# Performance work log

Hardware: AMD Instinct MI355X
Metric: run time of the kernel (lower is better)

Reference implementation:

```python
import jax, jax.numpy as jnp
import numpy as np

B, S, D, H, P = 2, 2048, 512, 8, 10  # batch, seq, d_model, heads, max_relative_position
DH = D // H
SCALE = float(np.sqrt(D))  # module uses sqrt(d_model) in relative branch


def _rel_indices(len_q, len_k, max_rel):
    rq = jnp.arange(len_q)
    rk = jnp.arange(len_k)
    dist = rk[None, :] - rq[:, None]
    return jnp.clip(dist, -max_rel, max_rel) + max_rel  # [len_q, len_k]


def setup_inputs() -> dict:
    key = jax.random.key(0)
    ks = jax.random.split(key, 12)
    init = lambda k, shp, s=0.02: (jax.random.normal(k, shp, dtype=jnp.float32) * s)
    return {
        "q": jax.random.normal(ks[0], (B, S, D), dtype=jnp.float32),
        "k": jax.random.normal(ks[1], (B, S, D), dtype=jnp.float32),
        "v": jax.random.normal(ks[2], (B, S, D), dtype=jnp.float32),
        "mask": jnp.ones((1, 1, S, S), dtype=jnp.int32),  # no-op in original (masked_fill result discarded)
        "Wq": init(ks[3], (D, D)), "bq": init(ks[4], (D,)),
        "Wk": init(ks[5], (D, D)), "bk": init(ks[6], (D,)),
        "Wv": init(ks[7], (D, D)), "bv": init(ks[8], (D,)),
        "W0": init(ks[9], (D, D)), "b0": init(ks[10], (D,)),
        "rel_k_table": init(ks[11], (2 * P + 1, DH), 0.02),
        "rel_v_table": init(jax.random.fold_in(key, 99), (2 * P + 1, DH), 0.02),
    }


def reference(q, k, v, mask, Wq, bq, Wk, bk, Wv, bv, W0, b0, rel_k_table, rel_v_table):
    # Projections (nn.Linear equivalent with weight stored as [in, out])
    query = q @ Wq + bq  # [B,S,D]
    key_ = k @ Wk + bk
    value = v @ Wv + bv

    qh = query.reshape(B, S, H, DH)  # [B,S,H,DH]
    kh = key_.reshape(B, S, H, DH)
    vh = value.reshape(B, S, H, DH)

    idx = _rel_indices(S, S, P)              # [S,S]
    rel_k = rel_k_table[idx]                 # [S,S,DH]
    rel_v = rel_v_table[idx]                 # [S,S,DH]

    normal_scores = jnp.einsum("bqhd,bkhd->bhqk", qh, kh)
    rel_scores = jnp.einsum("bqhd,qkd->bhqk", qh, rel_k)
    # NOTE: original relative branch applies NO softmax; mask is a no-op (masked_fill not in-place)
    scores = (normal_scores + rel_scores) / SCALE  # [B,H,S,S]

    weight1 = jnp.einsum("bhqk,bkhd->bhqd", scores, vh)
    weight2 = jnp.einsum("bhqk,qkd->bhqd", scores, rel_v)
    x = (weight1 + weight2).transpose(0, 2, 1, 3).reshape(B, S, D)
    return x @ W0 + b0
```

## Files before the change

### kernel.cpp

```cpp
#include <hip/hip_runtime.h>
#include <hip/hip_bf16.h>


typedef __attribute__((ext_vector_type(8)))  short  short8;
typedef __attribute__((ext_vector_type(4)))  short  short4v;
typedef __attribute__((ext_vector_type(16))) float  f32x16;
typedef __attribute__((ext_vector_type(8)))  __bf16 bf16x8;

#define DEV static __device__ __forceinline__

constexpr float INV_SCALE = 0.044194173824159216f;

DEV unsigned short f2bs(float f){ __hip_bfloat16 h = __float2bfloat16(f); unsigned short u; __builtin_memcpy(&u,&h,2); return u; }
DEV short f2b(float f){ return (short)f2bs(f); }
DEV float b2f(short s){ unsigned u = ((unsigned)(unsigned short)s)<<16; float f; __builtin_memcpy(&f,&u,4); return f; }
DEV bf16x8 ld8s(const short* p){ return __builtin_bit_cast(bf16x8, *(const short8*)p); }
DEV f32x16 z16(){ f32x16 z;
#pragma unroll
  for (int i=0;i<16;++i) z[i]=0.f;
  return z; }
DEV f32x16 mfma32(bf16x8 a, bf16x8 b, f32x16 c){ return __builtin_amdgcn_mfma_f32_32x32x16_bf16(a,b,c,0,0,0); }

template<bool AF32, bool OUTB16>
DEV void gemm_body(const void* A, const float* W, const float* bias, void* C,
                   int m0, int n0, short* Alds, short* Blds, short* Xt){
  const int tid = threadIdx.x, lane = tid&63, wid = tid>>6, lo5 = lane&31, hi = lane>>5;
  f32x16 acc0 = z16(), acc1 = z16();
  const int rr = tid>>3, c = tid&7;
  const int r2 = tid>>2, c4 = tid&3;
  const int kc = r2>>3, ko = r2&7;

  short8 avreg[4];
  short8 bv0r, bv1r;

  auto loadA = [&](int k0){
#pragma unroll
    for (int p=0;p<4;++p){
      const int row = p*32 + rr;
      if (AF32){
        const float* ap = (const float*)A + (size_t)(m0+row)*512 + k0 + c*8;
        float4 x = *(const float4*)ap; float4 y = *(const float4*)(ap+4);
        avreg[p] = short8{ f2b(x.x),f2b(x.y),f2b(x.z),f2b(x.w),
                           f2b(y.x),f2b(y.y),f2b(y.z),f2b(y.w) };
      } else {
        avreg[p] = *(const short8*)((const short*)A + (size_t)(m0+row)*512 + k0 + c*8);
      }
    }
  };
  auto loadB = [&](int k0){
    const float* wrow = W + (size_t)(k0+r2)*512 + n0 + c4*16;
    float4 f0 = *(const float4*)(wrow);
    float4 f1 = *(const float4*)(wrow+4);
    float4 f2 = *(const float4*)(wrow+8);
    float4 f3 = *(const float4*)(wrow+12);
    bv0r = short8{ f2b(f0.x),f2b(f0.y),f2b(f0.z),f2b(f0.w),
                   f2b(f1.x),f2b(f1.y),f2b(f1.z),f2b(f1.w) };
    bv1r = short8{ f2b(f2.x),f2b(f2.y),f2b(f2.z),f2b(f2.w),
                   f2b(f3.x),f2b(f3.y),f2b(f3.z),f2b(f3.w) };
  };

  loadA(0); loadB(0);
  for (int kt=0; kt<8; ++kt){
    __syncthreads();
    {
#pragma unroll
      for (int p=0;p<4;++p){
        const int row = p*32 + rr;
        *(short8*)&Alds[row*64 + ((c ^ (row&7))*8)] = avreg[p];
      }
#pragma unroll
      for (int e=0;e<16;++e){
        const int n = c4*16 + e;
        const short val = (e<8) ? bv0r[e] : bv1r[e-8];
        Blds[n*64 + ((kc ^ (n&7))*8) + ko] = val;
      }
    }
    __syncthreads();
    if (kt < 7){ loadA((kt+1)*64); loadB((kt+1)*64); }
#pragma unroll
    for (int da=0; da<4; ++da){
      const int arow = wid*32 + lo5;
      bf16x8 af = ld8s(&Alds[arow*64 + (((2*da+hi) ^ (arow&7))*8)]);
      const int b0r = lo5, b1r = 32+lo5;
      bf16x8 bf0 = ld8s(&Blds[b0r*64 + (((2*da+hi) ^ (b0r&7))*8)]);
      bf16x8 bf1 = ld8s(&Blds[b1r*64 + (((2*da+hi) ^ (b1r&7))*8)]);
      acc0 = mfma32(af, bf0, acc0);
      acc1 = mfma32(af, bf1, acc1);
    }
  }
  const float bv0 = bias[n0 + lo5], bv1 = bias[n0 + 32 + lo5];
#pragma unroll
  for (int r=0;r<16;++r){
    const int m = m0 + wid*32 + (r&3) + 8*(r>>2) + 4*hi;
    const float v0 = acc0[r] + bv0, v1 = acc1[r] + bv1;
    if (OUTB16){
      ((short*)C)[(size_t)m*512 + n0 + lo5]      = f2b(v0);
      ((short*)C)[(size_t)m*512 + n0 + 32 + lo5] = f2b(v1);
    } else {
      ((float*)C)[(size_t)m*512 + n0 + lo5]      = v0;
      ((float*)C)[(size_t)m*512 + n0 + 32 + lo5] = v1;
    }
  }
  if (Xt){
    __syncthreads();
#pragma unroll
    for (int r=0;r<16;++r){
      const int ml = wid*32 + (r&3) + 8*(r>>2) + 4*hi;
      Alds[ml*64 + lo5]      = f2b(acc0[r] + bv0);
      Alds[ml*64 + 32 + lo5] = f2b(acc1[r] + bv1);
    }
    __syncthreads();
    const int dh = tid & 63, chq = tid >> 6;
    short* xrow = Xt + (size_t)dh*2048 + chq*32;
#pragma unroll
    for (int cp=0; cp<4; ++cp){
      short8 t;
#pragma unroll
      for (int e=0;e<8;++e) t[e] = Alds[(chq*32 + cp*8 + e)*64 + dh];
      *(short8*)(xrow + cp*8) = t;
    }
  }
}

struct ProjArgs { const float* A[3]; const float* W[3]; const float* bias[3]; short* C[3]; short* XT[3]; };

__global__ __launch_bounds__(256) void proj_gemm(ProjArgs args){
  __shared__ short Alds[128*64];
  __shared__ short Blds[64*64];
  const int z = blockIdx.z;
  const int m0 = blockIdx.x*128, n0 = blockIdx.y*64;
  short* xt = nullptr;
  if (args.XT[z]){
    const int b = m0>>11, h = n0>>6, s0 = m0&2047;
    xt = args.XT[z] + ((size_t)(b*8+h)*64)*2048 + s0;
  }
  gemm_body<true,true>(args.A[z], args.W[z], args.bias[z], args.C[z],
                       m0, n0, Alds, Blds, xt);
}

__global__ __launch_bounds__(256) void out_gemm(const short* A, const float* W, const float* bias, float* C){
  __shared__ short Alds[128*64];
  __shared__ short Blds[64*64];
  gemm_body<false,false>(A, W, bias, C, blockIdx.x*128, blockIdx.y*64, Alds, Blds, nullptr);
}

__global__ __launch_bounds__(256) void kvpfx_kernel(const short* Kp, const short* Vp,
    const short* Kt, const short* Vt, float* KVpart, float* KP, float* VP){
  __shared__ float shmem[4*64*64];
  const int blk = blockIdx.x, tid = threadIdx.x;

  if (blk < 128){
    const int bh = blk>>3, ch = blk&7;
    const int lane = tid&63, wid = tid>>6, lo5 = lane&31, hi = lane>>5;
    const short* Ktb = Kt + (size_t)bh*64*2048;
    const short* Vtb = Vt + (size_t)bh*64*2048;
    f32x16 a00=z16(), a01=z16(), a10=z16(), a11=z16();
    const int sb = ch*256 + wid*64;
    for (int s = sb; s < sb+64; s += 16){
      bf16x8 ka = ld8s(Ktb + (size_t)lo5*2048 + s + hi*8);
      bf16x8 kb = ld8s(Ktb + (size_t)(32+lo5)*2048 + s + hi*8);
      bf16x8 va = ld8s(Vtb + (size_t)lo5*2048 + s + hi*8);
      bf16x8 vb = ld8s(Vtb + (size_t)(32+lo5)*2048 + s + hi*8);
      a00 = mfma32(ka, va, a00);
      a01 = mfma32(ka, vb, a01);
      a10 = mfma32(kb, va, a10);
      a11 = mfma32(kb, vb, a11);
    }
    float (*red)[64][64] = (float(*)[64][64])shmem;
#pragma unroll
    for (int r=0;r<16;++r){
      int ir = (r&3) + 8*(r>>2) + 4*hi;
      red[wid][ir][lo5]        = a00[r];
      red[wid][ir][32+lo5]     = a01[r];
      red[wid][32+ir][lo5]     = a10[r];
      red[wid][32+ir][32+lo5]  = a11[r];
    }
    __syncthreads();
    float* dst = KVpart + (size_t)(bh*8+ch)*4096;
    for (int e = tid; e < 4096; e += 256){
      int j = e>>6, i = e&63;
      dst[e] = red[0][i][j] + red[1][i][j] + red[2][i][j] + red[3][i][j];
    }
  } else {
    const int idx = blk - 128;
    const int bh = idx>>2, z = (idx>>1)&1, dhalf = idx&1;
    const int b = bh>>3, h = bh&7;
    const short* X = (z ? Vp : Kp) + (size_t)b*2048*512 + h*64 + dhalf*32;
    float* P = (z ? VP : KP) + (size_t)bh*2048*64 + dhalf*32;
    const int dg = tid & 3;
    const int ch = tid >> 2;
    float (*tot)[4][8] = (float(*)[4][8])shmem;

    const short* xp = X + (size_t)(ch*32)*512 + dg*8;
    float acc[8];
#pragma unroll
    for (int j=0;j<8;++j) acc[j]=0.f;
    for (int i=0;i<32;++i){
      short8 v = *(const short8*)(xp + (size_t)i*512);
#pragma unroll
      for (int j=0;j<8;++j) acc[j] += b2f(v[j]);
    }
#pragma unroll
    for (int j=0;j<8;++j) tot[ch][dg][j] = acc[j];
    __syncthreads();

    float run[8];
#pragma unroll
    for (int j=0;j<8;++j) run[j]=0.f;
    for (int cc=0; cc<ch; ++cc){
      float4 a = *(const float4*)&tot[cc][dg][0];
      float4 c4 = *(const float4*)&tot[cc][dg][4];
      run[0]+=a.x; run[1]+=a.y; run[2]+=a.z; run[3]+=a.w;
      run[4]+=c4.x; run[5]+=c4.y; run[6]+=c4.z; run[7]+=c4.w;
    }
    float* pp = P + (size_t)(ch*32)*64 + dg*8;
    for (int i=0;i<32;++i){
      short8 v = *(const short8*)(xp + (size_t)i*512);
#pragma unroll
      for (int j=0;j<8;++j) run[j] += b2f(v[j]);
      float4 o0 = { run[0], run[1], run[2], run[3] };
      float4 o1 = { run[4], run[5], run[6], run[7] };
      *(float4*)(pp + (size_t)i*64)     = o0;
      *(float4*)(pp + (size_t)i*64 + 4) = o1;
    }
  }
}

__global__ __launch_bounds__(256) void attn2_kernel(const short* Qp, const short* Kp,
    const short* Vt, const float* KVpart, const float* KP, const float* VP,
    const float* relk_g, const float* relv_g, short* xb){
  const int qt = blockIdx.x, bh = blockIdx.y;
  const int b = bh>>3, h = bh&7;
  const int tid = threadIdx.x, lane = tid&63, wid = tid>>6, lo5 = lane&31, hi = lane>>5;
  const int q0 = qt*128, qw = q0 + wid*32;

  __shared__ float Rq[128*21];
  __shared__ short CS[128*32];
  __shared__ short RVT[64*32];
  __shared__ short KVl[64*64];

  for (int i=tid; i<2048; i+=256) ((int*)CS)[i] = 0;
  for (int i=tid; i<2048; i+=256){
    int d = i>>5, j = i&31;
    RVT[d*32 + (j ^ ((d&3)<<3))] = (j<21) ? f2b(relv_g[j*64+d]) : (short)0;
  }

  {
    const int j = tid>>2, i0 = (tid&3)*16;
    float acc[16];
#pragma unroll
    for (int t=0;t<16;++t) acc[t]=0.f;
#pragma unroll
    for (int c=0;c<8;++c){
      const float* p = KVpart + (size_t)(bh*8+c)*4096 + j*64 + i0;
#pragma unroll
      for (int t4=0;t4<4;++t4){
        float4 v = *(const float4*)(p + t4*4);
        acc[t4*4+0]+=v.x; acc[t4*4+1]+=v.y; acc[t4*4+2]+=v.z; acc[t4*4+3]+=v.w;
      }
    }
#pragma unroll
    for (int half=0; half<2; ++half){
      short8 o;
#pragma unroll
      for (int e=0;e<8;++e) o[e] = f2b(acc[half*8+e]);
      const int chunk = (i0>>3) + half;
      *(short8*)&KVl[j*64 + ((chunk ^ (j&7))*8)] = o;
    }
  }

  bf16x8 qf[4];
  {
    const short* Qrow = Qp + (size_t)(b*2048 + qw + lo5)*512 + h*64 + hi*8;
#pragma unroll
    for (int da=0;da<4;++da) qf[da] = ld8s(Qrow + da*16);
  }

  {
    f32x16 rq = z16();
    const int jr = lo5 <= 20 ? lo5 : 20;
    const float* rp = relk_g + jr*64 + hi*8;
#pragma unroll
    for (int da=0;da<4;++da){
      const float* p = rp + da*16;
      float4 x = *(const float4*)p; float4 y = *(const float4*)(p+4);
      short8 rb = { f2b(x.x),f2b(x.y),f2b(x.z),f2b(x.w), f2b(y.x),f2b(y.y),f2b(y.z),f2b(y.w) };
      rq = mfma32(qf[da], __builtin_bit_cast(bf16x8, rb), rq);
    }
    if (lo5 <= 20){
#pragma unroll
      for (int r=0;r<16;++r){
        int qoff = (r&3) + 8*(r>>2) + 4*hi;
        Rq[(wid*32 + qoff)*21 + lo5] = rq[r];
      }
    }
  }
  __syncthreads();

  const int qrow = wid*32 + lo5;
  const int qg = q0 + qrow;

  f32x16 w1a = z16(), w1b = z16();

  {
#pragma unroll
    for (int c=0;c<4;++c){
      const int r0i = lo5, r1i = 32+lo5, ck = 2*c+hi;
      bf16x8 b0v = ld8s(&KVl[r0i*64 + ((ck ^ (r0i&7))*8)]);
      bf16x8 b1v = ld8s(&KVl[r1i*64 + ((ck ^ (r1i&7))*8)]);
      w1a = mfma32(qf[c], b0v, w1a);
      w1b = mfma32(qf[c], b1v, w1b);
    }
  }

  {
    const short* Vg = Vt + (size_t)bh*64*2048;
#pragma unroll
    for (int c=0;c<4;++c){
      const int kb = qw - 16 + c*16;
      const int kbse = kb + hi*8;
      const int jb = kbse - (qw + lo5) + 10;
      short8 av;
#pragma unroll
      for (int e=0;e<8;++e){
        int j = jb + e, kk = kbse + e;
        int jc = j < 1 ? 1 : (j > 19 ? 19 : j);
        float rv = Rq[qrow*21 + jc];
        bool ok = (j>=1) && (j<=19) && (kk>=0) && (kk<2048);
        av[e] = ok ? f2b(rv) : (short)0;
      }
      bf16x8 af = __builtin_bit_cast(bf16x8, av);
      const int kc = kb < 0 ? 0 : (kb > 2048-16 ? 2048-16 : kb);
      bf16x8 v0 = ld8s(Vg + (size_t)lo5*2048 + kc + hi*8);
      bf16x8 v1 = ld8s(Vg + (size_t)(32+lo5)*2048 + kc + hi*8);
      w1a = mfma32(af, v0, w1a);
      w1b = mfma32(af, v1, w1b);
    }
  }

  {
    const float* VPb = VP + (size_t)bh*2048*64;
    const float vt0 = VPb[(size_t)2047*64 + lo5];
    const float vt1 = VPb[(size_t)2047*64 + 32 + lo5];
#pragma unroll
    for (int r=0;r<16;++r){
      const int q_r = qw + (r&3) + 8*(r>>2) + 4*hi;
      const int ql = q_r - q0;
      const float r0q  = Rq[ql*21 + 0];
      const float r20q = Rq[ql*21 + 20];
      float p0=0.f, p1=0.f, s0=0.f, s1=0.f;
      if (q_r >= 10){
        const float* pr = VPb + (size_t)(q_r-10)*64;
        p0 = pr[lo5]; p1 = pr[32+lo5];
      }
      if (q_r <= 2037){
        const float* sr = VPb + (size_t)(q_r+9)*64;
        s0 = vt0 - sr[lo5]; s1 = vt1 - sr[32+lo5];
      }
      w1a[r] += r0q*p0 + r20q*s0;
      w1b[r] += r0q*p1 + r20q*s1;
    }
  }

  {
    const short* Kg = Kp + (size_t)b*2048*512 + h*64;
#pragma unroll
    for (int t3=0; t3<3; ++t3){
      const int kb = qw - 32 + t3*32;
      if (kb < 0 || kb >= 2048) continue;
      const short* Krow = Kg + (size_t)(kb + lo5)*512 + hi*8;
      f32x16 acc = z16();
#pragma unroll
      for (int da=0;da<4;++da) acc = mfma32(ld8s(Krow + da*16), qf[da], acc);
#pragma unroll
      for (int r=0;r<16;++r){
        const int krow = kb + (r&3) + 8*(r>>2) + 4*hi;
        const int j = krow - qg + 10;
        if (j >= 1 && j <= 19)
          CS[qrow*32 + (j ^ ((qrow&3)<<3))] = f2b(acc[r] + Rq[qrow*21 + j]);
      }
    }
  }

  {
    const int half = tid >> 7, q_loc = tid & 127;
    const int q_g2 = q0 + q_loc;
    const short* Qr = Qp + (size_t)(b*2048 + q_g2)*512 + h*64;
    const float* KPb = KP + (size_t)bh*2048*64;
    float val = 0.f;
    if (half == 0){
      if (q_g2 >= 10){
        const float* Pr = KPb + (size_t)(q_g2-10)*64;
        float dot = 0.f;
#pragma unroll
        for (int ii=0; ii<8; ++ii){
          short8 qv = *(const short8*)(Qr + ii*8);
          float4 p0 = *(const float4*)(Pr + ii*8);
          float4 p1 = *(const float4*)(Pr + ii*8 + 4);
          dot += b2f(qv[0])*p0.x + b2f(qv[1])*p0.y + b2f(qv[2])*p0.z + b2f(qv[3])*p0.w
               + b2f(qv[4])*p1.x + b2f(qv[5])*p1.y + b2f(qv[6])*p1.z + b2f(qv[7])*p1.w;
        }
        val = dot + (float)(q_g2 - 9) * Rq[q_loc*21 + 0];
      }
      CS[q_loc*32 + (0 ^ ((q_loc&3)<<3))] = f2b(val);
    } else {
      if (q_g2 <= 2037){
        const float* Pt = KPb + (size_t)2047*64;
        const float* Pr = KPb + (size_t)(q_g2+9)*64;
        float dot = 0.f;
#pragma unroll
        for (int ii=0; ii<8; ++ii){
          short8 qv = *(const short8*)(Qr + ii*8);
          float4 p0 = *(const float4*)(Pr + ii*8);
          float4 t0 = *(const float4*)(Pt + ii*8);
          float4 p1 = *(const float4*)(Pr + ii*8 + 4);
          float4 t1 = *(const float4*)(Pt + ii*8 + 4);
          dot += b2f(qv[0])*(t0.x-p0.x) + b2f(qv[1])*(t0.y-p0.y)
               + b2f(qv[2])*(t0.z-p0.z) + b2f(qv[3])*(t0.w-p0.w)
               + b2f(qv[4])*(t1.x-p1.x) + b2f(qv[5])*(t1.y-p1.y)
               + b2f(qv[6])*(t1.z-p1.z) + b2f(qv[7])*(t1.w-p1.w);
        }
        val = dot + (float)(2038 - q_g2) * Rq[q_loc*21 + 20];
      }
      CS[q_loc*32 + (20 ^ ((q_loc&3)<<3))] = f2b(val);
    }
  }
  __syncthreads();

  f32x16 w2a = z16(), w2b = z16();
#pragma unroll
  for (int c2=0;c2<2;++c2){
    const int arow = wid*32 + lo5;
    bf16x8 cf  = ld8s(&CS[arow*32 + ((16*c2 + 8*hi) ^ ((arow&3)<<3))]);
    const int d0 = lo5, d1 = 32 + lo5;
    bf16x8 rv0 = ld8s(&RVT[d0*32 + ((16*c2 + 8*hi) ^ ((d0&3)<<3))]);
    bf16x8 rv1 = ld8s(&RVT[d1*32 + ((16*c2 + 8*hi) ^ ((d1&3)<<3))]);
    w2a = mfma32(cf, rv0, w2a);
    w2b = mfma32(cf, rv1, w2b);
  }

#pragma unroll
  for (int r=0;r<16;++r){
    const int q_r = qw + (r&3) + 8*(r>>2) + 4*hi;
    const size_t o = ((size_t)b*2048 + q_r)*512 + h*64;
    xb[o + lo5]      = f2b((w1a[r] + w2a[r]) * INV_SCALE);
    xb[o + 32 + lo5] = f2b((w1b[r] + w2b[r]) * INV_SCALE);
  }
}

extern "C" void kernel_launch(void* const* d_in, const int* in_sizes, int n_in,
                              void* d_out, int out_size, void* d_ws, size_t ws_size,
                              hipStream_t stream) {
  (void)in_sizes; (void)n_in; (void)out_size; (void)ws_size;
  const float* q    = (const float*)d_in[0];
  const float* k    = (const float*)d_in[1];
  const float* v    = (const float*)d_in[2];
  const float* Wq   = (const float*)d_in[4];
  const float* bq   = (const float*)d_in[5];
  const float* Wk   = (const float*)d_in[6];
  const float* bk   = (const float*)d_in[7];
  const float* Wv   = (const float*)d_in[8];
  const float* bv   = (const float*)d_in[9];
  const float* W0   = (const float*)d_in[10];
  const float* b0   = (const float*)d_in[11];
  const float* relk = (const float*)d_in[12];
  const float* relv = (const float*)d_in[13];
  float* out = (float*)d_out;
  char* ws = (char*)d_ws;

  short* Qp  = (short*)(ws + ((size_t) 2<<20));
  short* Kp  = (short*)(ws + ((size_t) 6<<20));
  short* Vp  = (short*)(ws + ((size_t)10<<20));
  short* Vt  = (short*)(ws + ((size_t)14<<20));
  short* Kt  = (short*)(ws + ((size_t)18<<20));
  float* KVpart = (float*)(ws + ((size_t)22<<20));
  float* KP  = (float*)(ws + ((size_t)24<<20));
  float* VP  = (float*)(ws + ((size_t)32<<20));
  short* xb  = (short*)(ws + ((size_t)40<<20));

  ProjArgs pa = { {q, k, v}, {Wq, Wk, Wv}, {bq, bk, bv}, {Qp, Kp, Vp},
                  {nullptr, Kt, Vt} };
  proj_gemm<<<dim3(32,8,3), 256, 0, stream>>>(pa);

  kvpfx_kernel<<<192, 256, 0, stream>>>(Kp, Vp, Kt, Vt, KVpart, KP, VP);

  attn2_kernel<<<dim3(16,16), 256, 0, stream>>>(Qp, Kp, Vt, KVpart, KP, VP, relk, relv, xb);

  out_gemm<<<dim3(32,8), 256, 0, stream>>>(xb, W0, b0, out);
}
```

Baseline: 81.88 us.

## Fuse prefix, attention and output GEMM into one persistent kernel with grid barriers

Merges the three kernels that follow the projection GEMM into a single 256-block kernel. Software grid barriers built on atomic counters replace the kernel boundaries between stages, and the counters are zeroed by a memset before each launch. The goal is to remove launch overhead and the gaps between dependent kernels. In exchange, every block must be co-resident for the barriers to be safe, blocks spin-wait while others finish, and a shared 64KB LDS buffer may reduce occupancy.

```diff
diff --git a/kernel.cpp b/kernel.cpp
--- a/kernel.cpp
+++ b/kernel.cpp
@@ -20,6 +20,19 @@
   for (int i=0;i<16;++i) z[i]=0.f;
   return z; }
 DEV f32x16 mfma32(bf16x8 a, bf16x8 b, f32x16 c){ return __builtin_amdgcn_mfma_f32_32x32x16_bf16(a,b,c,0,0,0); }
+
+DEV void gridbar(unsigned* cnt, unsigned NB){
+  __syncthreads();
+  __threadfence();
+  if (threadIdx.x == 0){
+    __hip_atomic_fetch_add(cnt, 1u, __ATOMIC_ACQ_REL, __HIP_MEMORY_SCOPE_AGENT);
+    while (__hip_atomic_load(cnt, __ATOMIC_ACQUIRE, __HIP_MEMORY_SCOPE_AGENT) < NB){
+      __builtin_amdgcn_s_sleep(2);
+    }
+  }
+  __syncthreads();
+  __threadfence();
+}
 
 template<bool AF32, bool OUTB16>
 DEV void gemm_body(const void* A, const float* W, const float* bias, void* C,
@@ -138,313 +151,325 @@
                        m0, n0, Alds, Blds, xt);
 }
 
-__global__ __launch_bounds__(256) void out_gemm(const short* A, const float* W, const float* bias, float* C){
-  __shared__ short Alds[128*64];
-  __shared__ short Blds[64*64];
-  gemm_body<false,false>(A, W, bias, C, blockIdx.x*128, blockIdx.y*64, Alds, Blds, nullptr);
-}
-
-__global__ __launch_bounds__(256) void kvpfx_kernel(const short* Kp, const short* Vp,
-    const short* Kt, const short* Vt, float* KVpart, float* KP, float* VP){
-  __shared__ float shmem[4*64*64];
+struct TailArgs {
+  const short* Qp; const short* Kp; const short* Vp;
+  const short* Kt; const short* Vt;
+  float* KVpart; float* KP; float* VP;
+  const float* relk; const float* relv;
+  short* xb;
+  const float* W0; const float* b0; float* out;
+  unsigned* cnt;
+};
+
+__global__ __launch_bounds__(256) void tail_kernel(TailArgs a){
+  __shared__ char smem[65536];
   const int blk = blockIdx.x, tid = threadIdx.x;
-
-  if (blk < 128){
-    const int bh = blk>>3, ch = blk&7;
-    const int lane = tid&63, wid = tid>>6, lo5 = lane&31, hi = lane>>5;
-    const short* Ktb = Kt + (size_t)bh*64*2048;
-    const short* Vtb = Vt + (size_t)bh*64*2048;
-    f32x16 a00=z16(), a01=z16(), a10=z16(), a11=z16();
-    const int sb = ch*256 + wid*64;
-    for (int s = sb; s < sb+64; s += 16){
-      bf16x8 ka = ld8s(Ktb + (size_t)lo5*2048 + s + hi*8);
-      bf16x8 kb = ld8s(Ktb + (size_t)(32+lo5)*2048 + s + hi*8);
-      bf16x8 va = ld8s(Vtb + (size_t)lo5*2048 + s + hi*8);
-      bf16x8 vb = ld8s(Vtb + (size_t)(32+lo5)*2048 + s + hi*8);
-      a00 = mfma32(ka, va, a00);
-      a01 = mfma32(ka, vb, a01);
-      a10 = mfma32(kb, va, a10);
-      a11 = mfma32(kb, vb, a11);
-    }
-    float (*red)[64][64] = (float(*)[64][64])shmem;
-#pragma unroll
-    for (int r=0;r<16;++r){
-      int ir = (r&3) + 8*(r>>2) + 4*hi;
-      red[wid][ir][lo5]        = a00[r];
-      red[wid][ir][32+lo5]     = a01[r];
-      red[wid][32+ir][lo5]     = a10[r];
-      red[wid][32+ir][32+lo5]  = a11[r];
+  const int lane = tid&63, wid = tid>>6, lo5 = lane&31, hi = lane>>5;
+
+  if (blk < 192){
+    float* shmem = (float*)smem;
+    if (blk < 128){
+      const int bh = blk>>3, ch = blk&7;
+      const short* Ktb = a.Kt + (size_t)bh*64*2048;
+      const short* Vtb = a.Vt + (size_t)bh*64*2048;
+      f32x16 a00=z16(), a01=z16(), a10=z16(), a11=z16();
+      const int sb = ch*256 + wid*64;
+      for (int s = sb; s < sb+64; s += 16){
+        bf16x8 ka = ld8s(Ktb + (size_t)lo5*2048 + s + hi*8);
+        bf16x8 kb = ld8s(Ktb + (size_t)(32+lo5)*2048 + s + hi*8);
+        bf16x8 va = ld8s(Vtb + (size_t)lo5*2048 + s + hi*8);
+        bf16x8 vb = ld8s(Vtb + (size_t)(32+lo5)*2048 + s + hi*8);
+        a00 = mfma32(ka, va, a00);
+        a01 = mfma32(ka, vb, a01);
+        a10 = mfma32(kb, va, a10);
+        a11 = mfma32(kb, vb, a11);
+      }
+      float (*red)[64][64] = (float(*)[64][64])shmem;
+#pragma unroll
+      for (int r=0;r<16;++r){
+        int ir = (r&3) + 8*(r>>2) + 4*hi;
+        red[wid][ir][lo5]        = a00[r];
+        red[wid][ir][32+lo5]     = a01[r];
+        red[wid][32+ir][lo5]     = a10[r];
+        red[wid][32+ir][32+lo5]  = a11[r];
+      }
+      __syncthreads();
+      float* dst = a.KVpart + (size_t)blk*4096;
+      for (int e = tid; e < 4096; e += 256){
+        int j = e>>6, i = e&63;
+        dst[e] = red[0][i][j] + red[1][i][j] + red[2][i][j] + red[3][i][j];
+      }
+    } else {
+      const int idx = blk - 128;
+      const int bh = idx>>2, z = (idx>>1)&1, dhalf = idx&1;
+      const int b = bh>>3, h = bh&7;
+      const short* X = (z ? a.Vp : a.Kp) + (size_t)b*2048*512 + h*64 + dhalf*32;
+      float* P = (z ? a.VP : a.KP) + (size_t)bh*2048*64 + dhalf*32;
+      const int dg = tid & 3;
+      const int ch = tid >> 2;
+      float (*tot)[4][8] = (float(*)[4][8])smem;
+
+      const short* xp = X + (size_t)(ch*32)*512 + dg*8;
+      float acc[8];
+#pragma unroll
+      for (int j=0;j<8;++j) acc[j]=0.f;
+      for (int i=0;i<32;++i){
+        short8 v = *(const short8*)(xp + (size_t)i*512);
+#pragma unroll
+        for (int j=0;j<8;++j) acc[j] += b2f(v[j]);
+      }
+#pragma unroll
+      for (int j=0;j<8;++j) tot[ch][dg][j] = acc[j];
+      __syncthreads();
+
+      float run[8];
+#pragma unroll
+      for (int j=0;j<8;++j) run[j]=0.f;
+      for (int cc=0; cc<ch; ++cc){
+        float4 a4 = *(const float4*)&tot[cc][dg][0];
+        float4 c4v = *(const float4*)&tot[cc][dg][4];
+        run[0]+=a4.x; run[1]+=a4.y; run[2]+=a4.z; run[3]+=a4.w;
+        run[4]+=c4v.x; run[5]+=c4v.y; run[6]+=c4v.z; run[7]+=c4v.w;
+      }
+      float* pp = P + (size_t)(ch*32)*64 + dg*8;
+      for (int i=0;i<32;++i){
+        short8 v = *(const short8*)(xp + (size_t)i*512);
+#pragma unroll
+        for (int j=0;j<8;++j) run[j] += b2f(v[j]);
+        float4 o0 = { run[0], run[1], run[2], run[3] };
+        float4 o1 = { run[4], run[5], run[6], run[7] };
+        *(float4*)(pp + (size_t)i*64)     = o0;
+        *(float4*)(pp + (size_t)i*64 + 4) = o1;
+      }
+    }
+  }
+  gridbar(a.cnt + 0, 256);
+
+  {
+    const int qt = blk>>4, bh = blk&15;
+    const int b = bh>>3, h = bh&7;
+    const int q0 = qt*128, qw = q0 + wid*32;
+
+    float* Rq  = (float*)smem;
+    short* CS  = (short*)(smem + 10752);
+    short* RVT = (short*)(smem + 10752 + 8192);
+    short* KVl = (short*)(smem + 10752 + 8192 + 4096);
+
+    for (int i=tid; i<2048; i+=256) ((int*)CS)[i] = 0;
+    for (int i=tid; i<2048; i+=256){
+      int d = i>>5, j = i&31;
+      RVT[d*32 + (j ^ ((d&3)<<3))] = (j<21) ? f2b(a.relv[j*64+d]) : (short)0;
+    }
+
+    {
+      const int j = tid>>2, i0 = (tid&3)*16;
+      float acc[16];
+#pragma unroll
+      for (int t=0;t<16;++t) acc[t]=0.f;
+#pragma unroll
+      for (int c=0;c<8;++c){
+        const float* p = a.KVpart + (size_t)(bh*8+c)*4096 + j*64 + i0;
+#pragma unroll
+        for (int t4=0;t4<4;++t4){
+          float4 v = *(const float4*)(p + t4*4);
+          acc[t4*4+0]+=v.x; acc[t4*4+1]+=v.y; acc[t4*4+2]+=v.z; acc[t4*4+3]+=v.w;
+        }
+      }
+#pragma unroll
+      for (int half=0; half<2; ++half){
+        short8 o;
+#pragma unroll
+        for (int e=0;e<8;++e) o[e] = f2b(acc[half*8+e]);
+        const int chunk = (i0>>3) + half;
+        *(short8*)&KVl[j*64 + ((chunk ^ (j&7))*8)] = o;
+      }
+    }
+
+    bf16x8 qf[4];
+    {
+      const short* Qrow = a.Qp + (size_t)(b*2048 + qw + lo5)*512 + h*64 + hi*8;
+#pragma unroll
+      for (int da=0;da<4;++da) qf[da] = ld8s(Qrow + da*16);
+    }
+
+    {
+      f32x16 rq = z16();
+      const int jr = lo5 <= 20 ? lo5 : 20;
+      const float* rp = a.relk + jr*64 + hi*8;
+#pragma unroll
+      for (int da=0;da<4;++da){
+        const float* p = rp + da*16;
+        float4 x = *(const float4*)p; float4 y = *(const float4*)(p+4);
+        short8 rb = { f2b(x.x),f2b(x.y),f2b(x.z),f2b(x.w), f2b(y.x),f2b(y.y),f2b(y.z),f2b(y.w) };
+        rq = mfma32(qf[da], __builtin_bit_cast(bf16x8, rb), rq);
+      }
+      if (lo5 <= 20){
+#pragma unroll
+        for (int r=0;r<16;++r){
+          int qoff = (r&3) + 8*(r>>2) + 4*hi;
+          Rq[(wid*32 + qoff)*21 + lo5] = rq[r];
+        }
+      }
     }
     __syncthreads();
-    float* dst = KVpart + (size_t)(bh*8+ch)*4096;
-    for (int e = tid; e < 4096; e += 256){
-      int j = e>>6, i = e&63;
-      dst[e] = red[0][i][j] + red[1][i][j] + red[2][i][j] + red[3][i][j];
-    }
-  } else {
-    const int idx = blk - 128;
-    const int bh = idx>>2, z = (idx>>1)&1, dhalf = idx&1;
-    const int b = bh>>3, h = bh&7;
-    const short* X = (z ? Vp : Kp) + (size_t)b*2048*512 + h*64 + dhalf*32;
-    float* P = (z ? VP : KP) + (size_t)bh*2048*64 + dhalf*32;
-    const int dg = tid & 3;
-    const int ch = tid >> 2;
-    float (*tot)[4][8] = (float(*)[4][8])shmem;
-
-    const short* xp = X + (size_t)(ch*32)*512 + dg*8;
-    float acc[8];
-#pragma unroll
-    for (int j=0;j<8;++j) acc[j]=0.f;
-    for (int i=0;i<32;++i){
-      short8 v = *(const short8*)(xp + (size_t)i*512);
-#pragma unroll
-      for (int j=0;j<8;++j) acc[j] += b2f(v[j]);
-    }
-#pragma unroll
-    for (int j=0;j<8;++j) tot[ch][dg][j] = acc[j];
+
+    const int qrow = wid*32 + lo5;
+    const int qg = q0 + qrow;
+
+    f32x16 w1a = z16(), w1b = z16();
+
+    {
+#pragma unroll
+      for (int c=0;c<4;++c){
+        const int r0i = lo5, r1i = 32+lo5, ck = 2*c+hi;
+        bf16x8 b0v = ld8s(&KVl[r0i*64 + ((ck ^ (r0i&7))*8)]);
+        bf16x8 b1v = ld8s(&KVl[r1i*64 + ((ck ^ (r1i&7))*8)]);
+        w1a = mfma32(qf[c], b0v, w1a);
+        w1b = mfma32(qf[c], b1v, w1b);
+      }
+    }
+
+    {
+      const short* Vg = a.Vt + (size_t)bh*64*2048;
+#pragma unroll
+      for (int c=0;c<4;++c){
+        const int kb = qw - 16 + c*16;
+        const int kbse = kb + hi*8;
+        const int jb = kbse - (qw + lo5) + 10;
+        short8 av;
+#pragma unroll
+        for (int e=0;e<8;++e){
+          int j = jb + e, kk = kbse + e;
+          int jc = j < 1 ? 1 : (j > 19 ? 19 : j);
+          float rv = Rq[qrow*21 + jc];
+          bool ok = (j>=1) && (j<=19) && (kk>=0) && (kk<2048);
+          av[e] = ok ? f2b(rv) : (short)0;
+        }
+        bf16x8 af = __builtin_bit_cast(bf16x8, av);
+        const int kcx = kb < 0 ? 0 : (kb > 2048-16 ? 2048-16 : kb);
+        bf16x8 v0 = ld8s(Vg + (size_t)lo5*2048 + kcx + hi*8);
+        bf16x8 v1 = ld8s(Vg + (size_t)(32+lo5)*2048 + kcx + hi*8);
+        w1a = mfma32(af, v0, w1a);
+        w1b = mfma32(af, v1, w1b);
+      }
+    }
+
+    {
+      const float* VPb = a.VP + (size_t)bh*2048*64;
+      const float vt0 = VPb[(size_t)2047*64 + lo5];
+      const float vt1 = VPb[(size_t)2047*64 + 32 + lo5];
+#pragma unroll
+      for (int r=0;r<16;++r){
+        const int q_r = qw + (r&3) + 8*(r>>2) + 4*hi;
+        const int ql = q_r - q0;
+        const float r0q  = Rq[ql*21 + 0];
+        const float r20q = Rq[ql*21 + 20];
+        float p0=0.f, p1=0.f, s0=0.f, s1=0.f;
+        if (q_r >= 10){
+          const float* pr = VPb + (size_t)(q_r-10)*64;
+          p0 = pr[lo5]; p1 = pr[32+lo5];
+        }
+        if (q_r <= 2037){
+          const float* sr = VPb + (size_t)(q_r+9)*64;
+          s0 = vt0 - sr[lo5]; s1 = vt1 - sr[32+lo5];
+        }
+        w1a[r] += r0q*p0 + r20q*s0;
+        w1b[r] += r0q*p1 + r20q*s1;
+      }
+    }
+
+    {
+      const short* Kg = a.Kp + (size_t)b*2048*512 + h*64;
+#pragma unroll
+      for (int t3=0; t3<3; ++t3){
+        const int kb = qw - 32 + t3*32;
+        if (kb < 0 || kb >= 2048) continue;
+        const short* Krow = Kg + (size_t)(kb + lo5)*512 + hi*8;
+        f32x16 acc = z16();
+#pragma unroll
+        for (int da=0;da<4;++da) acc = mfma32(ld8s(Krow + da*16), qf[da], acc);
+#pragma unroll
+        for (int r=0;r<16;++r){
+          const int krow = kb + (r&3) + 8*(r>>2) + 4*hi;
+          const int j = krow - qg + 10;
+          if (j >= 1 && j <= 19)
+            CS[qrow*32 + (j ^ ((qrow&3)<<3))] = f2b(acc[r] + Rq[qrow*21 + j]);
+        }
+      }
+    }
+
+    {
+      const int half = tid >> 7, q_loc = tid & 127;
+      const int q_g2 = q0 + q_loc;
+      const short* Qr = a.Qp + (size_t)(b*2048 + q_g2)*512 + h*64;
+      const float* KPb = a.KP + (size_t)bh*2048*64;
+      float val = 0.f;
+      if (half == 0){
+        if (q_g2 >= 10){
+          const float* Pr = KPb + (size_t)(q_g2-10)*64;
+          float dot = 0.f;
+#pragma unroll
+          for (int ii=0; ii<8; ++ii){
+            short8 qv = *(const short8*)(Qr + ii*8);
+            float4 p0 = *(const float4*)(Pr + ii*8);
+            float4 p1 = *(const float4*)(Pr + ii*8 + 4);
+            dot += b2f(qv[0])*p0.x + b2f(qv[1])*p0.y + b2f(qv[2])*p0.z + b2f(qv[3])*p0.w
+                 + b2f(qv[4])*p1.x + b2f(qv[5])*p1.y + b2f(qv[6])*p1.z + b2f(qv[7])*p1.w;
+          }
+          val = dot + (float)(q_g2 - 9) * Rq[q_loc*21 + 0];
+        }
+        CS[q_loc*32 + (0 ^ ((q_loc&3)<<3))] = f2b(val);
+      } else {
+        if (q_g2 <= 2037){
+          const float* Pt = KPb + (size_t)2047*64;
+          const float* Pr = KPb + (size_t)(q_g2+9)*64;
+          float dot = 0.f;
+#pragma unroll
+          for (int ii=0; ii<8; ++ii){
+            short8 qv = *(const short8*)(Qr + ii*8);
+            float4 p0 = *(const float4*)(Pr + ii*8);
+            float4 t0 = *(const float4*)(Pt + ii*8);
+            float4 p1 = *(const float4*)(Pr + ii*8 + 4);
+            float4 t1 = *(const float4*)(Pt + ii*8 + 4);
+            dot += b2f(qv[0])*(t0.x-p0.x) + b2f(qv[1])*(t0.y-p0.y)
+                 + b2f(qv[2])*(t0.z-p0.z) + b2f(qv[3])*(t0.w-p0.w)
+                 + b2f(qv[4])*(t1.x-p1.x) + b2f(qv[5])*(t1.y-p1.y)
+                 + b2f(qv[6])*(t1.z-p1.z) + b2f(qv[7])*(t1.w-p1.w);
+          }
+          val = dot + (float)(2038 - q_g2) * Rq[q_loc*21 + 20];
+        }
+        CS[q_loc*32 + (20 ^ ((q_loc&3)<<3))] = f2b(val);
+      }
+    }
     __syncthreads();
 
-    float run[8];
-#pragma unroll
-    for (int j=0;j<8;++j) run[j]=0.f;
-    for (int cc=0; cc<ch; ++cc){
-      float4 a = *(const float4*)&tot[cc][dg][0];
-      float4 c4 = *(const float4*)&tot[cc][dg][4];
-      run[0]+=a.x; run[1]+=a.y; run[2]+=a.z; run[3]+=a.w;
-      run[4]+=c4.x; run[5]+=c4.y; run[6]+=c4.z; run[7]+=c4.w;
-    }
-    float* pp = P + (size_t)(ch*32)*64 + dg*8;
-    for (int i=0;i<32;++i){
-      short8 v = *(const short8*)(xp + (size_t)i*512);
-#pragma unroll
-      for (int j=0;j<8;++j) run[j] += b2f(v[j]);
-      float4 o0 = { run[0], run[1], run[2], run[3] };
-      float4 o1 = { run[4], run[5], run[6], run[7] };
-      *(float4*)(pp + (size_t)i*64)     = o0;
-      *(float4*)(pp + (size_t)i*64 + 4) = o1;
-    }
-  }
-}
-
-__global__ __launch_bounds__(256) void attn2_kernel(const short* Qp, const short* Kp,
-    const short* Vt, const float* KVpart, const float* KP, const float* VP,
-    const float* relk_g, const float* relv_g, short* xb){
-  const int qt = blockIdx.x, bh = blockIdx.y;
-  const int b = bh>>3, h = bh&7;
-  const int tid = threadIdx.x, lane = tid&63, wid = tid>>6, lo5 = lane&31, hi = lane>>5;
-  const int q0 = qt*128, qw = q0 + wid*32;
-
-  __shared__ float Rq[128*21];
-  __shared__ short CS[128*32];
-  __shared__ short RVT[64*32];
-  __shared__ short KVl[64*64];
-
-  for (int i=tid; i<2048; i+=256) ((int*)CS)[i] = 0;
-  for (int i=tid; i<2048; i+=256){
-    int d = i>>5, j = i&31;
-    RVT[d*32 + (j ^ ((d&3)<<3))] = (j<21) ? f2b(relv_g[j*64+d]) : (short)0;
-  }
-
-  {
-    const int j = tid>>2, i0 = (tid&3)*16;
-    float acc[16];
-#pragma unroll
-    for (int t=0;t<16;++t) acc[t]=0.f;
-#pragma unroll
-    for (int c=0;c<8;++c){
-      const float* p = KVpart + (size_t)(bh*8+c)*4096 + j*64 + i0;
-#pragma unroll
-      for (int t4=0;t4<4;++t4){
-        float4 v = *(const float4*)(p + t4*4);
-        acc[t4*4+0]+=v.x; acc[t4*4+1]+=v.y; acc[t4*4+2]+=v.z; acc[t4*4+3]+=v.w;
-      }
-    }
-#pragma unroll
-    for (int half=0; half<2; ++half){
-      short8 o;
-#pragma unroll
-      for (int e=0;e<8;++e) o[e] = f2b(acc[half*8+e]);
-      const int chunk = (i0>>3) + half;
-      *(short8*)&KVl[j*64 + ((chunk ^ (j&7))*8)] = o;
-    }
-  }
-
-  bf16x8 qf[4];
-  {
-    const short* Qrow = Qp + (size_t)(b*2048 + qw + lo5)*512 + h*64 + hi*8;
-#pragma unroll
-    for (int da=0;da<4;++da) qf[da] = ld8s(Qrow + da*16);
-  }
-
-  {
-    f32x16 rq = z16();
-    const int jr = lo5 <= 20 ? lo5 : 20;
-    const float* rp = relk_g + jr*64 + hi*8;
-#pragma unroll
-    for (int da=0;da<4;++da){
-      const float* p = rp + da*16;
-      float4 x = *(const float4*)p; float4 y = *(const float4*)(p+4);
-      short8 rb = { f2b(x.x),f2b(x.y),f2b(x.z),f2b(x.w), f2b(y.x),f2b(y.y),f2b(y.z),f2b(y.w) };
-      rq = mfma32(qf[da], __builtin_bit_cast(bf16x8, rb), rq);
-    }
-    if (lo5 <= 20){
-#pragma unroll
-      for (int r=0;r<16;++r){
-        int qoff = (r&3) + 8*(r>>2) + 4*hi;
-        Rq[(wid*32 + qoff)*21 + lo5] = rq[r];
-      }
-    }
-  }
-  __syncthreads();
-
-  const int qrow = wid*32 + lo5;
-  const int qg = q0 + qrow;
-
-  f32x16 w1a = z16(), w1b = z16();
-
-  {
-#pragma unroll
-    for (int c=0;c<4;++c){
-      const int r0i = lo5, r1i = 32+lo5, ck = 2*c+hi;
-      bf16x8 b0v = ld8s(&KVl[r0i*64 + ((ck ^ (r0i&7))*8)]);
-      bf16x8 b1v = ld8s(&KVl[r1i*64 + ((ck ^ (r1i&7))*8)]);
-      w1a = mfma32(qf[c], b0v, w1a);
-      w1b = mfma32(qf[c], b1v, w1b);
-    }
-  }
-
-  {
-    const short* Vg = Vt + (size_t)bh*64*2048;
-#pragma unroll
-    for (int c=0;c<4;++c){
-      const int kb = qw - 16 + c*16;
-      const int kbse = kb + hi*8;
-      const int jb = kbse - (qw + lo5) + 10;
-      short8 av;
-#pragma unroll
-      for (int e=0;e<8;++e){
-        int j = jb + e, kk = kbse + e;
-        int jc = j < 1 ? 1 : (j > 19 ? 19 : j);
-        float rv = Rq[qrow*21 + jc];
-        bool ok = (j>=1) && (j<=19) && (kk>=0) && (kk<2048);
-        av[e] = ok ? f2b(rv) : (short)0;
-      }
-      bf16x8 af = __builtin_bit_cast(bf16x8, av);
-      const int kc = kb < 0 ? 0 : (kb > 2048-16 ? 2048-16 : kb);
-      bf16x8 v0 = ld8s(Vg + (size_t)lo5*2048 + kc + hi*8);
-      bf16x8 v1 = ld8s(Vg + (size_t)(32+lo5)*2048 + kc + hi*8);
-      w1a = mfma32(af, v0, w1a);
-      w1b = mfma32(af, v1, w1b);
-    }
-  }
-
-  {
-    const float* VPb = VP + (size_t)bh*2048*64;
-    const float vt0 = VPb[(size_t)2047*64 + lo5];
-    const float vt1 = VPb[(size_t)2047*64 + 32 + lo5];
+    f32x16 w2a = z16(), w2b = z16();
+#pragma unroll
+    for (int c2=0;c2<2;++c2){
+      const int arow = wid*32 + lo5;
+      bf16x8 cf  = ld8s(&CS[arow*32 + ((16*c2 + 8*hi) ^ ((arow&3)<<3))]);
+      const int d0 = lo5, d1 = 32 + lo5;
+      bf16x8 rv0 = ld8s(&RVT[d0*32 + ((16*c2 + 8*hi) ^ ((d0&3)<<3))]);
+      bf16x8 rv1 = ld8s(&RVT[d1*32 + ((16*c2 + 8*hi) ^ ((d1&3)<<3))]);
+      w2a = mfma32(cf, rv0, w2a);
+      w2b = mfma32(cf, rv1, w2b);
+    }
+
 #pragma unroll
     for (int r=0;r<16;++r){
       const int q_r = qw + (r&3) + 8*(r>>2) + 4*hi;
-      const int ql = q_r - q0;
-      const float r0q  = Rq[ql*21 + 0];
-      const float r20q = Rq[ql*21 + 20];
-      float p0=0.f, p1=0.f, s0=0.f, s1=0.f;
-      if (q_r >= 10){
-        const float* pr = VPb + (size_t)(q_r-10)*64;
-        p0 = pr[lo5]; p1 = pr[32+lo5];
-      }
-      if (q_r <= 2037){
-        const float* sr = VPb + (size_t)(q_r+9)*64;
-        s0 = vt0 - sr[lo5]; s1 = vt1 - sr[32+lo5];
-      }
-      w1a[r] += r0q*p0 + r20q*s0;
-      w1b[r] += r0q*p1 + r20q*s1;
-    }
-  }
+      const size_t o = ((size_t)b*2048 + q_r)*512 + h*64;
+      a.xb[o + lo5]      = f2b((w1a[r] + w2a[r]) * INV_SCALE);
+      a.xb[o + 32 + lo5] = f2b((w1b[r] + w2b[r]) * INV_SCALE);
+    }
+  }
+  gridbar(a.cnt + 1, 256);
 
   {
-    const short* Kg = Kp + (size_t)b*2048*512 + h*64;
-#pragma unroll
-    for (int t3=0; t3<3; ++t3){
-      const int kb = qw - 32 + t3*32;
-      if (kb < 0 || kb >= 2048) continue;
-      const short* Krow = Kg + (size_t)(kb + lo5)*512 + hi*8;
-      f32x16 acc = z16();
-#pragma unroll
-      for (int da=0;da<4;++da) acc = mfma32(ld8s(Krow + da*16), qf[da], acc);
-#pragma unroll
-      for (int r=0;r<16;++r){
-        const int krow = kb + (r&3) + 8*(r>>2) + 4*hi;
-        const int j = krow - qg + 10;
-        if (j >= 1 && j <= 19)
-          CS[qrow*32 + (j ^ ((qrow&3)<<3))] = f2b(acc[r] + Rq[qrow*21 + j]);
-      }
-    }
-  }
-
-  {
-    const int half = tid >> 7, q_loc = tid & 127;
-    const int q_g2 = q0 + q_loc;
-    const short* Qr = Qp + (size_t)(b*2048 + q_g2)*512 + h*64;
-    const float* KPb = KP + (size_t)bh*2048*64;
-    float val = 0.f;
-    if (half == 0){
-      if (q_g2 >= 10){
-        const float* Pr = KPb + (size_t)(q_g2-10)*64;
-        float dot = 0.f;
-#pragma unroll
-        for (int ii=0; ii<8; ++ii){
-          short8 qv = *(const short8*)(Qr + ii*8);
-          float4 p0 = *(const float4*)(Pr + ii*8);
-          float4 p1 = *(const float4*)(Pr + ii*8 + 4);
-          dot += b2f(qv[0])*p0.x + b2f(qv[1])*p0.y + b2f(qv[2])*p0.z + b2f(qv[3])*p0.w
-               + b2f(qv[4])*p1.x + b2f(qv[5])*p1.y + b2f(qv[6])*p1.z + b2f(qv[7])*p1.w;
-        }
-        val = dot + (float)(q_g2 - 9) * Rq[q_loc*21 + 0];
-      }
-      CS[q_loc*32 + (0 ^ ((q_loc&3)<<3))] = f2b(val);
-    } else {
-      if (q_g2 <= 2037){
-        const float* Pt = KPb + (size_t)2047*64;
-        const float* Pr = KPb + (size_t)(q_g2+9)*64;
-        float dot = 0.f;
-#pragma unroll
-        for (int ii=0; ii<8; ++ii){
-          short8 qv = *(const short8*)(Qr + ii*8);
-          float4 p0 = *(const float4*)(Pr + ii*8);
-          float4 t0 = *(const float4*)(Pt + ii*8);
-          float4 p1 = *(const float4*)(Pr + ii*8 + 4);
-          float4 t1 = *(const float4*)(Pt + ii*8 + 4);
-          dot += b2f(qv[0])*(t0.x-p0.x) + b2f(qv[1])*(t0.y-p0.y)
-               + b2f(qv[2])*(t0.z-p0.z) + b2f(qv[3])*(t0.w-p0.w)
-               + b2f(qv[4])*(t1.x-p1.x) + b2f(qv[5])*(t1.y-p1.y)
-               + b2f(qv[6])*(t1.z-p1.z) + b2f(qv[7])*(t1.w-p1.w);
-        }
-        val = dot + (float)(2038 - q_g2) * Rq[q_loc*21 + 20];
-      }
-      CS[q_loc*32 + (20 ^ ((q_loc&3)<<3))] = f2b(val);
-    }
-  }
-  __syncthreads();
-
-  f32x16 w2a = z16(), w2b = z16();
-#pragma unroll
-  for (int c2=0;c2<2;++c2){
-    const int arow = wid*32 + lo5;
-    bf16x8 cf  = ld8s(&CS[arow*32 + ((16*c2 + 8*hi) ^ ((arow&3)<<3))]);
-    const int d0 = lo5, d1 = 32 + lo5;
-    bf16x8 rv0 = ld8s(&RVT[d0*32 + ((16*c2 + 8*hi) ^ ((d0&3)<<3))]);
-    bf16x8 rv1 = ld8s(&RVT[d1*32 + ((16*c2 + 8*hi) ^ ((d1&3)<<3))]);
-    w2a = mfma32(cf, rv0, w2a);
-    w2b = mfma32(cf, rv1, w2b);
-  }
-
-#pragma unroll
-  for (int r=0;r<16;++r){
-    const int q_r = qw + (r&3) + 8*(r>>2) + 4*hi;
-    const size_t o = ((size_t)b*2048 + q_r)*512 + h*64;
-    xb[o + lo5]      = f2b((w1a[r] + w2a[r]) * INV_SCALE);
-    xb[o + 32 + lo5] = f2b((w1b[r] + w2b[r]) * INV_SCALE);
+    short* Alds = (short*)smem;
+    short* Blds = (short*)(smem + 16384);
+    const int m0 = (blk>>3)*128, n0 = (blk&7)*64;
+    gemm_body<false,false>(a.xb, a.W0, a.b0, a.out, m0, n0, Alds, Blds, nullptr);
   }
 }
 
@@ -468,6 +493,7 @@
   float* out = (float*)d_out;
   char* ws = (char*)d_ws;
 
+  unsigned* cnt = (unsigned*)(ws + ((size_t)1<<20));
   short* Qp  = (short*)(ws + ((size_t) 2<<20));
   short* Kp  = (short*)(ws + ((size_t) 6<<20));
   short* Vp  = (short*)(ws + ((size_t)10<<20));
@@ -478,13 +504,12 @@
   float* VP  = (float*)(ws + ((size_t)32<<20));
   short* xb  = (short*)(ws + ((size_t)40<<20));
 
+  hipMemsetAsync(cnt, 0, 16, stream);
+
   ProjArgs pa = { {q, k, v}, {Wq, Wk, Wv}, {bq, bk, bv}, {Qp, Kp, Vp},
                   {nullptr, Kt, Vt} };
   proj_gemm<<<dim3(32,8,3), 256, 0, stream>>>(pa);
 
-  kvpfx_kernel<<<192, 256, 0, stream>>>(Kp, Vp, Kt, Vt, KVpart, KP, VP);
-
-  attn2_kernel<<<dim3(16,16), 256, 0, stream>>>(Qp, Kp, Vt, KVpart, KP, VP, relk, relv, xb);
-
-  out_gemm<<<dim3(32,8), 256, 0, stream>>>(xb, W0, b0, out);
+  TailArgs ta = { Qp, Kp, Vp, Kt, Vt, KVpart, KP, VP, relk, relv, xb, W0, b0, out, cnt };
+  tail_kernel<<<256, 256, 0, stream>>>(ta);
 }
```

New measurement: 269.5 us. +229.2%, slower.
